# Performance work log

Measured on AMD Instinct MI355X. Metric: run time of the kernel, lower is better.

The kernel has to match this reference:

```python
import jax, jax.numpy as jnp
import numpy as np

# dims: N batch, O out_channels, CI in_channels, H=W vertices, R rank
N, O, CI, H, R = 8, 32, 16, 512, 8


def setup_inputs() -> dict:
    key = jax.random.key(0)
    kx, kw, kb = jax.random.split(key, 3)
    X = jax.random.normal(kx, (N, CI, H, H), dtype=jnp.float32)
    # learnable left generator (right generator aliases it under symmetry=True)
    weight_L = jax.random.normal(kw, (O, CI, H, R), dtype=jnp.float32) * 0.02
    fan_in = CI * H * R  # torch fan_in for a (O, CI, H, R) weight
    bound = 1.0 / np.sqrt(fan_in)
    bias = jax.random.uniform(kb, (O,), dtype=jnp.float32, minval=-bound, maxval=bound)
    # coupling='split': fixed (non-learnable) +/-1 diagonal coupling, first O//2 channels negative
    coupling = jnp.ones((O, CI, R, 1), dtype=jnp.float32).at[: O // 2].multiply(-1.0)
    return {"X": X, "weight_L": weight_L, "bias": bias, "coupling": coupling}


def reference(X, weight_L, bias, coupling):
    # --- template expansion: T[o,c] = L diag(coupling) L^T  (symmetric, low-rank) ---
    # coupling: (O,CI,R,1) -> per-rank sign broadcast over the rank axis of L
    Lc = weight_L * coupling[..., 0][..., None, :]            # (O,CI,H,R)
    T = jnp.einsum('ochr,ocwr->ochw', Lc, weight_L)           # (O,CI,H,W)
    # --- crosshair similarity, with the in_channel sum pulled inside ---
    P = jnp.einsum('nchw,ochw->nohw', X, T)                   # (N,O,H,W)
    out = P.sum(-1, keepdims=True) + P.sum(-2, keepdims=True) - P
    out = out + bias[None, :, None, None]
    # --- delete diagonal ---
    eye = jnp.eye(out.shape[-1], dtype=out.dtype)
    return out * (1.0 - eye)
```

## Files before the change

kernel.cpp:

```cpp
#include <hip/hip_runtime.h>
#include <cstdint>
#include <cstddef>
#include <utility>

#define Ndim 8
#define Odim 32
#define Cdim 16
#define Hdim 512
#define Rdim 8
#define TW 64
#define TH 4
#define NBW (Hdim/TW)
#define NBH (Hdim/TH)
#define HHsz ((size_t)Hdim*Hdim)

typedef _Float16 half2_t __attribute__((ext_vector_type(2)));
typedef unsigned int u32x4 __attribute__((ext_vector_type(4)));

union U16 { u32x4 u; half2_t h[4]; };

template <class F, int... Is>
__device__ __forceinline__ void unroll_impl(F&& f, std::integer_sequence<int, Is...>) {
    (f(std::integral_constant<int, Is>{}), ...);
}
template <int N, class F>
__device__ __forceinline__ void unrollN(F&& f) {
    unroll_impl(static_cast<F&&>(f), std::make_integer_sequence<int, N>{});
}

__device__ __forceinline__ half2_t pk(float a, float b) {
    half2_t h; h[0] = (_Float16)a; h[1] = (_Float16)b; return h;
}

#if defined(__has_builtin)
#if __has_builtin(__builtin_amdgcn_fdot2)
#define HAVE_FDOT2 1
#endif
#endif

__device__ __forceinline__ float fdot2f(half2_t a, half2_t b, float acc) {
#ifdef HAVE_FDOT2
    return __builtin_amdgcn_fdot2(a, b, acc, false);
#else
    return acc + (float)a[0] * (float)b[0] + (float)a[1] * (float)b[1];
#endif
}

__device__ __forceinline__ void stage16(const u32x4* g, u32x4* l) {
    __builtin_amdgcn_global_load_lds(
        (const __attribute__((address_space(1))) uint32_t*)g,
        (__attribute__((address_space(3))) uint32_t*)l, 16, 0, 0);
}

template<int CTRL>
__device__ __forceinline__ float dppadd(float v) {
    return v + __int_as_float(__builtin_amdgcn_update_dpp(
        0, __float_as_int(v), CTRL, 0xf, 0xf, true));
}
__device__ __forceinline__ float wave_sum63(float v) {
    v = dppadd<0xB1>(v);
    v = dppadd<0x4E>(v);
    v = dppadd<0x141>(v);
    v = dppadd<0x140>(v);
    v = dppadd<0x142>(v);
    v = dppadd<0x143>(v);
    return v;
}

__global__ __launch_bounds__(256)
void sylo_prep(const float* __restrict__ L, const float* __restrict__ coup,
               u32x4* __restrict__ lsigT, u32x4* __restrict__ lraw)
{
    int row = blockIdx.x * 256 + threadIdx.x;
    int oc = row >> 9, h = row & 511;
    int o = oc >> 4, c = oc & 15;
    const float4* lp = (const float4*)(L + (size_t)row * Rdim);
    const float4* cp = (const float4*)(coup + (size_t)oc * Rdim);
    float4 l0 = lp[0], l1 = lp[1];
    float4 c0 = cp[0], c1 = cp[1];
    U16 s, r;
    s.h[0] = pk(l0.x * c0.x, l0.y * c0.y); s.h[1] = pk(l0.z * c0.z, l0.w * c0.w);
    s.h[2] = pk(l1.x * c1.x, l1.y * c1.y); s.h[3] = pk(l1.z * c1.z, l1.w * c1.w);
    r.h[0] = pk(l0.x, l0.y); r.h[1] = pk(l0.z, l0.w);
    r.h[2] = pk(l1.x, l1.y); r.h[3] = pk(l1.z, l1.w);
    lsigT[((size_t)o * Hdim + h) * Cdim + c] = s.u;
    lraw[row] = r.u;
}

__global__ __launch_bounds__(256)
void sylo_xprep(const float* __restrict__ X, u32x4* __restrict__ Xh)
{
    int cid = blockIdx.x * 256 + threadIdx.x;
    int pxl = cid & 63;
    int k = (cid >> 6) & 15;
    size_t px = (size_t)(cid >> 10) * 64 + pxl;
    U16 v;
    unrollN<4>([&](auto ii) {
        constexpr int i = decltype(ii)::value;
        int pr = 4 * k + i;
        int cp = pr >> 3, n = pr & 7;
        float a = X[(size_t)(n * Cdim + 2 * cp)     * HHsz + px];
        float b = X[(size_t)(n * Cdim + 2 * cp + 1) * HHsz + px];
        v.h[i] = pk(a, b);
    });
    Xh[cid] = v.u;
}

template<int XH>
__device__ __forceinline__ void load_x(U16 (&xr)[16], const u32x4* __restrict__ Xh,
                                       const float* __restrict__ Xg,
                                       int hh, int bw, int j)
{
    if constexpr (XH) {
        const size_t base = ((size_t)hh * NBW + bw) * 1024 + j;
        unrollN<16>([&](auto ki) {
            constexpr int k = decltype(ki)::value;
            xr[k].u = Xh[base + k * 64];
        });
    } else {
        const size_t q = (size_t)hh * Hdim + bw * TW + j;
        unrollN<8>([&](auto cpi) {
            constexpr int cp = decltype(cpi)::value;
            unrollN<8>([&](auto ni) {
                constexpr int n = decltype(ni)::value;
                constexpr int idx = cp * 8 + n;
                xr[idx >> 2].h[idx & 3] = pk(Xg[(size_t)(n * Cdim + 2 * cp) * HHsz + q],
                                             Xg[(size_t)(n * Cdim + 2 * cp + 1) * HHsz + q]);
            });
            __builtin_amdgcn_sched_barrier(0);
        });
    }
    asm volatile("" :
        "+v"(xr[0].u), "+v"(xr[1].u), "+v"(xr[2].u), "+v"(xr[3].u),
        "+v"(xr[4].u), "+v"(xr[5].u), "+v"(xr[6].u), "+v"(xr[7].u),
        "+v"(xr[8].u), "+v"(xr[9].u), "+v"(xr[10].u), "+v"(xr[11].u),
        "+v"(xr[12].u), "+v"(xr[13].u), "+v"(xr[14].u), "+v"(xr[15].u));
}

__device__ __forceinline__ void stage_tile(const u32x4* __restrict__ lraw, int o,
                                           int w0, int j, int iw, u32x4 (&buf)[Cdim][TW])
{
    unrollN<4>([&](auto ki) {
        constexpr int k = decltype(ki)::value;
        int c = iw * 4 + k;
        stage16(lraw + ((size_t)(o * Cdim + c) * Hdim + w0 + j), &buf[c][0]);
    });
}
__device__ __forceinline__ void stage_tile_raw(const float* __restrict__ Lg, int o,
                                               int w0, int tid, u32x4 (&buf)[Cdim][TW])
{
    unrollN<4>([&](auto ki) {
        constexpr int k = decltype(ki)::value;
        int e = tid + k * 256, c = e >> 6, w = e & 63;
        const float4* gp = (const float4*)(Lg + ((size_t)(o * Cdim + c) * Hdim + w0 + w) * Rdim);
        float4 l0 = gp[0], l1 = gp[1];
        U16 t;
        t.h[0] = pk(l0.x, l0.y); t.h[1] = pk(l0.z, l0.w);
        t.h[2] = pk(l1.x, l1.y); t.h[3] = pk(l1.z, l1.w);
        buf[c][w] = t.u;
    });
}

template<int LP>
__device__ __forceinline__ void compute_p(
    int o, int ruh, int j, const u32x4 (&lwb)[Cdim][TW],
    const u32x4* __restrict__ lsigT, const float* __restrict__ Lg,
    const float* __restrict__ coupg, const U16 (&xr)[16], float (&p)[Ndim])
{
    unrollN<8>([&](auto ni) { p[decltype(ni)::value] = 0.f; });
    unrollN<8>([&](auto cpi) {
        constexpr int cp = decltype(cpi)::value;
        float tv0 = 0.f, tv1 = 0.f;
        unrollN<2>([&](auto hi) {
            constexpr int hf = decltype(hi)::value;
            constexpr int c = 2 * cp + hf;
            U16 A, B;
            if constexpr (LP) {
                A.u = lsigT[((size_t)o * Hdim + ruh) * Cdim + c];
            } else {
                const float4* a0 = (const float4*)(Lg + ((size_t)(o * Cdim + c) * Hdim + ruh) * Rdim);
                const float4* cpp = (const float4*)(coupg + (size_t)(o * Cdim + c) * Rdim);
                float4 l0 = a0[0], l1 = a0[1];
                float4 c0 = cpp[0], c1 = cpp[1];
                A.h[0] = pk(l0.x * c0.x, l0.y * c0.y); A.h[1] = pk(l0.z * c0.z, l0.w * c0.w);
                A.h[2] = pk(l1.x * c1.x, l1.y * c1.y); A.h[3] = pk(l1.z * c1.z, l1.w * c1.w);
            }
            B.u = lwb[c][j];
            float t = 0.f;
            unrollN<4>([&](auto ri) {
                constexpr int r = decltype(ri)::value;
                t = fdot2f(A.h[r], B.h[r], t);
            });
            if constexpr (hf == 0) tv0 = t; else tv1 = t;
        });
        half2_t t2 = pk(tv0, tv1);
        unrollN<8>([&](auto ni) {
            constexpr int n = decltype(ni)::value;
            constexpr int idx = cp * 8 + n;
            p[n] = fdot2f(t2, xr[idx >> 2].h[idx & 3], p[n]);
        });
        if constexpr (cp == 1 || cp == 3 || cp == 5)
            __builtin_amdgcn_sched_barrier(0);
    });
}

template<int XH, int LP, int DET>
__global__ __launch_bounds__(256, 4)
void sylo_p0(const float* __restrict__ Xg, const float* __restrict__ Lg,
             const float* __restrict__ coupg,
             const u32x4* __restrict__ Xh, const u32x4* __restrict__ lsigT,
             const u32x4* __restrict__ lraw,
             float* __restrict__ rsp, float* __restrict__ csp,
             float* __restrict__ rs, float* __restrict__ cs)
{
    const int tid = threadIdx.x;
    const int j = tid & 63, iw = tid >> 6;
    const int bw = blockIdx.x, bh = blockIdx.y;
    const int w0 = bw * TW, h0 = bh * TH;
    const int hh = h0 + iw;
    const size_t S = (size_t)Ndim * Odim * Hdim;

    __shared__ __align__(16) u32x4 lw[2][Cdim][TW];
    __shared__ float csl[TH][Ndim][TW];

    U16 xr[16];
    load_x<XH>(xr, Xh, Xg, hh, bw, j);
    const int ruh = __builtin_amdgcn_readfirstlane(hh);

    if (LP) stage_tile(lraw, 0, w0, j, iw, lw[0]);
    __syncthreads();

    for (int o = 0; o < Odim; ++o) {
        const int cur = LP ? (o & 1) : 0;
        if (LP) {
            if (o + 1 < Odim) stage_tile(lraw, o + 1, w0, j, iw, lw[cur ^ 1]);
        } else {
            stage_tile_raw(Lg, o, w0, tid, lw[0]);
            __syncthreads();
        }

        float p[Ndim];
        compute_p<LP>(o, ruh, j, lw[cur], lsigT, Lg, coupg, xr, p);

        unrollN<8>([&](auto ni) {
            constexpr int n = decltype(ni)::value;
            float r = wave_sum63(p[n]);
            if (j == 63) {
                size_t i0 = (size_t)(n * Odim + o) * Hdim + hh;
                if (DET) rsp[(size_t)bw * S + i0] = r;
                else atomicAdd(&rs[i0], r);
            }
            csl[iw][n][j] = p[n];
        });
        __syncthreads();
        unrollN<2>([&](auto ki) {
            constexpr int k = decltype(ki)::value;
            int f = tid + k * 256;
            int n = f >> 6, jj = f & 63;
            float v = csl[0][n][jj] + csl[1][n][jj] + csl[2][n][jj] + csl[3][n][jj];
            size_t idx = (size_t)(n * Odim + o) * Hdim + w0 + jj;
            if (DET) csp[(size_t)bh * S + idx] = v;
            else atomicAdd(&cs[idx], v);
        });
        __syncthreads();
    }
}

template<int XH, int LP>
__global__ __launch_bounds__(256, 4)
void sylo_p1(const float* __restrict__ Xg, const float* __restrict__ Lg,
             const float* __restrict__ coupg, const float* __restrict__ biasg,
             const u32x4* __restrict__ Xh, const u32x4* __restrict__ lsigT,
             const u32x4* __restrict__ lraw,
             float* __restrict__ outg,
             const float* __restrict__ rs, const float* __restrict__ cs)
{
    const int tid = threadIdx.x;
    const int j = tid & 63, iw = tid >> 6;
    const int bw = blockIdx.x, bh = blockIdx.y;
    const int w0 = bw * TW, h0 = bh * TH;
    const int hh = h0 + iw, ww = w0 + j;

    __shared__ __align__(16) u32x4 lw[2][Cdim][TW];

    U16 xr[16];
    load_x<XH>(xr, Xh, Xg, hh, bw, j);
    const int ruh = __builtin_amdgcn_readfirstlane(hh);

    if (LP) stage_tile(lraw, 0, w0, j, iw, lw[0]);
    __syncthreads();

    for (int o = 0; o < Odim; ++o) {
        const int cur = LP ? (o & 1) : 0;
        if (LP) {
            if (o + 1 < Odim) stage_tile(lraw, o + 1, w0, j, iw, lw[cur ^ 1]);
        } else {
            stage_tile_raw(Lg, o, w0, tid, lw[0]);
            __syncthreads();
        }

        float p[Ndim];
        compute_p<LP>(o, ruh, j, lw[cur], lsigT, Lg, coupg, xr, p);

        float bb = biasg[o];
        unrollN<8>([&](auto ni) {
            constexpr int n = decltype(ni)::value;
            size_t i0 = (size_t)(n * Odim + o) * Hdim;
            float rv = rs[i0 + (size_t)ruh];
            float cv = cs[i0 + ww];
            float v = rv + cv - p[n] + bb;
            if (hh == ww) v = 0.f;
            outg[(i0 + hh) * Hdim + ww] = v;
        });
        __syncthreads();
    }
}

__global__ __launch_bounds__(256)
void sylo_reduce(const float* __restrict__ rsp, const float* __restrict__ csp,
                 float* __restrict__ rs, float* __restrict__ cs)
{
    int t = blockIdx.x * 256 + threadIdx.x;
    const size_t S = (size_t)Ndim * Odim * Hdim;
    float a = 0.f;
    #pragma unroll
    for (int k = 0; k < NBW; ++k) a += rsp[(size_t)k * S + t];
    rs[t] = a;
    float b = 0.f;
    #pragma unroll 16
    for (int k = 0; k < NBH; ++k) b += csp[(size_t)k * S + t];
    cs[t] = b;
}

extern "C" void kernel_launch(void* const* d_in, const int* in_sizes, int n_in,
                              void* d_out, int out_size, void* d_ws, size_t ws_size,
                              hipStream_t stream)
{
    const float* X    = (const float*)d_in[0];
    const float* L    = (const float*)d_in[1];
    const float* bias = (const float*)d_in[2];
    const float* coup = (const float*)d_in[3];
    float* out = (float*)d_out;

    const size_t S    = (size_t)Ndim * Odim * Hdim;
    const size_t NL16 = (size_t)Odim * Cdim * Hdim;
    const size_t NXH  = HHsz * 16;
    const size_t need0 = NL16 * 16 * 2 + NXH * 16 + (size_t)(NBW + NBH) * S * 4 + 2 * S * 4;
    const size_t need1 = NL16 * 16 * 2 + NXH * 16 + 2 * S * 4;
    dim3 grid(NBW, NBH), blk(256);

    if (ws_size >= need0) {
        u32x4* lsigT = (u32x4*)d_ws;
        u32x4* lraw  = lsigT + NL16;
        u32x4* Xh    = lraw + NL16;
        float* rsp = (float*)(Xh + NXH);
        float* csp = rsp + (size_t)NBW * S;
        float* rs  = csp + (size_t)NBH * S;
        float* cs  = rs + S;
        sylo_prep<<<dim3(1024), blk, 0, stream>>>(L, coup, lsigT, lraw);
        sylo_xprep<<<dim3(16384), blk, 0, stream>>>(X, Xh);
        sylo_p0<1,1,1><<<grid, blk, 0, stream>>>(X, L, coup, Xh, lsigT, lraw, rsp, csp, rs, cs);
        sylo_reduce<<<dim3(512), blk, 0, stream>>>(rsp, csp, rs, cs);
        sylo_p1<1,1><<<grid, blk, 0, stream>>>(X, L, coup, bias, Xh, lsigT, lraw, out, rs, cs);
    } else if (ws_size >= need1) {
        u32x4* lsigT = (u32x4*)d_ws;
        u32x4* lraw  = lsigT + NL16;
        u32x4* Xh    = lraw + NL16;
        float* rs = (float*)(Xh + NXH);
        float* cs = rs + S;
        hipMemsetAsync(rs, 0, 2 * S * sizeof(float), stream);
        sylo_prep<<<dim3(1024), blk, 0, stream>>>(L, coup, lsigT, lraw);
        sylo_xprep<<<dim3(16384), blk, 0, stream>>>(X, Xh);
        sylo_p0<1,1,0><<<grid, blk, 0, stream>>>(X, L, coup, Xh, lsigT, lraw, nullptr, nullptr, rs, cs);
        sylo_p1<1,1><<<grid, blk, 0, stream>>>(X, L, coup, bias, Xh, lsigT, lraw, out, rs, cs);
    } else {
        float* rs = (float*)d_ws;
        float* cs = rs + S;
        hipMemsetAsync(rs, 0, 2 * S * sizeof(float), stream);
        sylo_p0<0,0,0><<<grid, blk, 0, stream>>>(X, L, coup, nullptr, nullptr, nullptr, nullptr, nullptr, rs, cs);
        sylo_p1<0,0><<<grid, blk, 0, stream>>>(X, L, coup, bias, nullptr, nullptr, nullptr, out, rs, cs);
    }
}
```

Baseline: 322.2 us.

## Store fp16 P from first pass and replace recompute pass with streaming epilogue

The first pass now writes the per-pixel P values, packed to fp16 with round-toward-zero conversion, into a workspace buffer. A simple streaming kernel then reads them back to build the output, so the second pass no longer recomputes P. The separate X-prep kernel is folded into the first pass, which writes a block-local fp16 X layout that is reused while iterating over output channels. The deterministic partial-sum reduction path is dropped in favour of atomics. In exchange the code adds a large extra fp16 write and read of P, rounds P to fp16 before the final subtraction, and makes the row and column sums non-deterministic.

```diff
diff --git a/kernel.cpp b/kernel.cpp
--- a/kernel.cpp
+++ b/kernel.cpp
@@ -15,9 +15,11 @@
 #define HHsz ((size_t)Hdim*Hdim)
 
 typedef _Float16 half2_t __attribute__((ext_vector_type(2)));
+typedef __fp16 fp16x2_t __attribute__((ext_vector_type(2)));
 typedef unsigned int u32x4 __attribute__((ext_vector_type(4)));
 
 union U16 { u32x4 u; half2_t h[4]; };
+union UPK { fp16x2_t f; half2_t h; unsigned int u; };
 
 template <class F, int... Is>
 __device__ __forceinline__ void unroll_impl(F&& f, std::integer_sequence<int, Is...>) {
@@ -33,10 +35,22 @@
 }
 
 #if defined(__has_builtin)
+#if __has_builtin(__builtin_amdgcn_cvt_pkrtz)
+#define HAVE_PKRTZ 1
+#endif
 #if __has_builtin(__builtin_amdgcn_fdot2)
 #define HAVE_FDOT2 1
 #endif
 #endif
+
+__device__ __forceinline__ half2_t pkz(float a, float b) {
+#ifdef HAVE_PKRTZ
+    UPK u; u.f = __builtin_amdgcn_cvt_pkrtz(a, b);
+    return u.h;
+#else
+    return pk(a, b);
+#endif
+}
 
 __device__ __forceinline__ float fdot2f(half2_t a, half2_t b, float acc) {
 #ifdef HAVE_FDOT2
@@ -87,56 +101,6 @@
     lraw[row] = r.u;
 }
 
-__global__ __launch_bounds__(256)
-void sylo_xprep(const float* __restrict__ X, u32x4* __restrict__ Xh)
-{
-    int cid = blockIdx.x * 256 + threadIdx.x;
-    int pxl = cid & 63;
-    int k = (cid >> 6) & 15;
-    size_t px = (size_t)(cid >> 10) * 64 + pxl;
-    U16 v;
-    unrollN<4>([&](auto ii) {
-        constexpr int i = decltype(ii)::value;
-        int pr = 4 * k + i;
-        int cp = pr >> 3, n = pr & 7;
-        float a = X[(size_t)(n * Cdim + 2 * cp)     * HHsz + px];
-        float b = X[(size_t)(n * Cdim + 2 * cp + 1) * HHsz + px];
-        v.h[i] = pk(a, b);
-    });
-    Xh[cid] = v.u;
-}
-
-template<int XH>
-__device__ __forceinline__ void load_x(U16 (&xr)[16], const u32x4* __restrict__ Xh,
-                                       const float* __restrict__ Xg,
-                                       int hh, int bw, int j)
-{
-    if constexpr (XH) {
-        const size_t base = ((size_t)hh * NBW + bw) * 1024 + j;
-        unrollN<16>([&](auto ki) {
-            constexpr int k = decltype(ki)::value;
-            xr[k].u = Xh[base + k * 64];
-        });
-    } else {
-        const size_t q = (size_t)hh * Hdim + bw * TW + j;
-        unrollN<8>([&](auto cpi) {
-            constexpr int cp = decltype(cpi)::value;
-            unrollN<8>([&](auto ni) {
-                constexpr int n = decltype(ni)::value;
-                constexpr int idx = cp * 8 + n;
-                xr[idx >> 2].h[idx & 3] = pk(Xg[(size_t)(n * Cdim + 2 * cp) * HHsz + q],
-                                             Xg[(size_t)(n * Cdim + 2 * cp + 1) * HHsz + q]);
-            });
-            __builtin_amdgcn_sched_barrier(0);
-        });
-    }
-    asm volatile("" :
-        "+v"(xr[0].u), "+v"(xr[1].u), "+v"(xr[2].u), "+v"(xr[3].u),
-        "+v"(xr[4].u), "+v"(xr[5].u), "+v"(xr[6].u), "+v"(xr[7].u),
-        "+v"(xr[8].u), "+v"(xr[9].u), "+v"(xr[10].u), "+v"(xr[11].u),
-        "+v"(xr[12].u), "+v"(xr[13].u), "+v"(xr[14].u), "+v"(xr[15].u));
-}
-
 __device__ __forceinline__ void stage_tile(const u32x4* __restrict__ lraw, int o,
                                            int w0, int j, int iw, u32x4 (&buf)[Cdim][TW])
 {
@@ -161,15 +125,31 @@
     });
 }
 
-template<int LP>
-__device__ __forceinline__ void compute_p(
-    int o, int ruh, int j, const u32x4 (&lwb)[Cdim][TW],
+template<int XH, int LP>
+__device__ __forceinline__ void compute_core(
+    int o, int ruh, int j, int tid,
+    const u32x4 (&lwb)[Cdim][TW], const u32x4* xsl,
+    const float* __restrict__ Xg, size_t q,
     const u32x4* __restrict__ lsigT, const float* __restrict__ Lg,
-    const float* __restrict__ coupg, const U16 (&xr)[16], float (&p)[Ndim])
+    const float* __restrict__ coupg, float (&p)[Ndim])
 {
     unrollN<8>([&](auto ni) { p[decltype(ni)::value] = 0.f; });
+    unsigned xofs = 0;
+    if constexpr (XH) { asm volatile("" : "+v"(xofs)); }
     unrollN<8>([&](auto cpi) {
         constexpr int cp = decltype(cpi)::value;
+        U16 x0, x1;
+        if constexpr (XH) {
+            x0.u = xsl[xofs + (2 * cp) * 256 + tid];
+            x1.u = xsl[xofs + (2 * cp + 1) * 256 + tid];
+        } else {
+            unrollN<4>([&](auto ni) { constexpr int n = decltype(ni)::value;
+                x0.h[n] = pk(Xg[(size_t)(n * Cdim + 2 * cp) * HHsz + q],
+                             Xg[(size_t)(n * Cdim + 2 * cp + 1) * HHsz + q]); });
+            unrollN<4>([&](auto ni) { constexpr int n = decltype(ni)::value;
+                x1.h[n] = pk(Xg[(size_t)((n + 4) * Cdim + 2 * cp) * HHsz + q],
+                             Xg[(size_t)((n + 4) * Cdim + 2 * cp + 1) * HHsz + q]); });
+        }
         float tv0 = 0.f, tv1 = 0.f;
         unrollN<2>([&](auto hi) {
             constexpr int hf = decltype(hi)::value;
@@ -194,62 +174,84 @@
             if constexpr (hf == 0) tv0 = t; else tv1 = t;
         });
         half2_t t2 = pk(tv0, tv1);
-        unrollN<8>([&](auto ni) {
-            constexpr int n = decltype(ni)::value;
-            constexpr int idx = cp * 8 + n;
-            p[n] = fdot2f(t2, xr[idx >> 2].h[idx & 3], p[n]);
-        });
+        unrollN<4>([&](auto ni) { constexpr int n = decltype(ni)::value;
+            p[n] = fdot2f(t2, x0.h[n], p[n]); });
+        unrollN<4>([&](auto ni) { constexpr int n = decltype(ni)::value;
+            p[n + 4] = fdot2f(t2, x1.h[n], p[n + 4]); });
         if constexpr (cp == 1 || cp == 3 || cp == 5)
             __builtin_amdgcn_sched_barrier(0);
     });
 }
 
-template<int XH, int LP, int DET>
+template<int BXH, int XH, int LP, int PF>
 __global__ __launch_bounds__(256, 4)
 void sylo_p0(const float* __restrict__ Xg, const float* __restrict__ Lg,
              const float* __restrict__ coupg,
-             const u32x4* __restrict__ Xh, const u32x4* __restrict__ lsigT,
-             const u32x4* __restrict__ lraw,
-             float* __restrict__ rsp, float* __restrict__ csp,
-             float* __restrict__ rs, float* __restrict__ cs)
+             const u32x4* __restrict__ lsigT, const u32x4* __restrict__ lraw,
+             u32x4* __restrict__ xh, u32x4* __restrict__ pf,
+             float* __restrict__ rs, float* __restrict__ cs,
+             int obase, int ocount)
 {
     const int tid = threadIdx.x;
     const int j = tid & 63, iw = tid >> 6;
     const int bw = blockIdx.x, bh = blockIdx.y;
-    const int w0 = bw * TW, h0 = bh * TH;
-    const int hh = h0 + iw;
-    const size_t S = (size_t)Ndim * Odim * Hdim;
+    const int w0 = bw * TW;
+    const int hh = bh * TH + iw, ww = w0 + j;
+    const size_t q = (size_t)hh * Hdim + ww;
 
     __shared__ __align__(16) u32x4 lw[2][Cdim][TW];
     __shared__ float csl[TH][Ndim][TW];
 
-    U16 xr[16];
-    load_x<XH>(xr, Xh, Xg, hh, bw, j);
+    u32x4* xsl = nullptr;
+    if constexpr (XH) xsl = xh + (size_t)(bh * NBW + bw) * 4096;
+
+    if constexpr (BXH) {
+        unrollN<16>([&](auto ki) {
+            constexpr int k = decltype(ki)::value;
+            U16 v;
+            unrollN<4>([&](auto ii) {
+                constexpr int i = decltype(ii)::value;
+                constexpr int pr = 4 * k + i;
+                constexpr int cp = pr >> 3, n = pr & 7;
+                v.h[i] = pk(Xg[(size_t)(n * Cdim + 2 * cp) * HHsz + q],
+                            Xg[(size_t)(n * Cdim + 2 * cp + 1) * HHsz + q]);
+            });
+            xsl[k * 256 + tid] = v.u;
+            if constexpr (k == 3 || k == 7 || k == 11) __builtin_amdgcn_sched_barrier(0);
+        });
+    }
+
     const int ruh = __builtin_amdgcn_readfirstlane(hh);
 
-    if (LP) stage_tile(lraw, 0, w0, j, iw, lw[0]);
+    if (LP) stage_tile(lraw, obase, w0, j, iw, lw[0]);
     __syncthreads();
 
-    for (int o = 0; o < Odim; ++o) {
-        const int cur = LP ? (o & 1) : 0;
+    for (int oo = 0; oo < ocount; ++oo) {
+        const int o = obase + oo;
+        const int cur = LP ? (oo & 1) : 0;
         if (LP) {
-            if (o + 1 < Odim) stage_tile(lraw, o + 1, w0, j, iw, lw[cur ^ 1]);
+            if (oo + 1 < ocount) stage_tile(lraw, o + 1, w0, j, iw, lw[cur ^ 1]);
         } else {
             stage_tile_raw(Lg, o, w0, tid, lw[0]);
             __syncthreads();
         }
 
         float p[Ndim];
-        compute_p<LP>(o, ruh, j, lw[cur], lsigT, Lg, coupg, xr, p);
+        compute_core<XH, LP>(o, ruh, j, tid, lw[cur], xsl, Xg, q, lsigT, Lg, coupg, p);
+
+        if constexpr (PF) {
+            U16 pv;
+            unrollN<4>([&](auto ki) {
+                constexpr int k = decltype(ki)::value;
+                pv.h[k] = pkz(p[2 * k], p[2 * k + 1]);
+            });
+            pf[((size_t)oo * Hdim + hh) * Hdim + ww] = pv.u;
+        }
 
         unrollN<8>([&](auto ni) {
             constexpr int n = decltype(ni)::value;
             float r = wave_sum63(p[n]);
-            if (j == 63) {
-                size_t i0 = (size_t)(n * Odim + o) * Hdim + hh;
-                if (DET) rsp[(size_t)bw * S + i0] = r;
-                else atomicAdd(&rs[i0], r);
-            }
+            if (j == 63) atomicAdd(&rs[(size_t)(n * Odim + o) * Hdim + hh], r);
             csl[iw][n][j] = p[n];
         });
         __syncthreads();
@@ -258,78 +260,74 @@
             int f = tid + k * 256;
             int n = f >> 6, jj = f & 63;
             float v = csl[0][n][jj] + csl[1][n][jj] + csl[2][n][jj] + csl[3][n][jj];
-            size_t idx = (size_t)(n * Odim + o) * Hdim + w0 + jj;
-            if (DET) csp[(size_t)bh * S + idx] = v;
-            else atomicAdd(&cs[idx], v);
+            atomicAdd(&cs[(size_t)(n * Odim + o) * Hdim + w0 + jj], v);
         });
         __syncthreads();
     }
 }
 
-template<int XH, int LP>
-__global__ __launch_bounds__(256, 4)
-void sylo_p1(const float* __restrict__ Xg, const float* __restrict__ Lg,
-             const float* __restrict__ coupg, const float* __restrict__ biasg,
-             const u32x4* __restrict__ Xh, const u32x4* __restrict__ lsigT,
-             const u32x4* __restrict__ lraw,
-             float* __restrict__ outg,
-             const float* __restrict__ rs, const float* __restrict__ cs)
+__global__ __launch_bounds__(256)
+void sylo_p1s(const u32x4* __restrict__ pf, const float* __restrict__ rs,
+              const float* __restrict__ cs, const float* __restrict__ biasg,
+              float* __restrict__ outg, int obase, int OL)
 {
     const int tid = threadIdx.x;
     const int j = tid & 63, iw = tid >> 6;
     const int bw = blockIdx.x, bh = blockIdx.y;
-    const int w0 = bw * TW, h0 = bh * TH;
-    const int hh = h0 + iw, ww = w0 + j;
-
+    const int hh = bh * TH + iw, ww = bw * TW + j;
+    const int ruh = __builtin_amdgcn_readfirstlane(hh);
+
+    for (int oo = 0; oo < OL; ++oo) {
+        const int oc = blockIdx.z * OL + oo;
+        const int o = obase + oc;
+        U16 pv;
+        pv.u = pf[((size_t)oc * Hdim + hh) * Hdim + ww];
+        float bb = biasg[o];
+        unrollN<4>([&](auto ki) {
+            constexpr int k = decltype(ki)::value;
+            constexpr int n0 = 2 * k, n1 = 2 * k + 1;
+            float pa = (float)pv.h[k][0], pb = (float)pv.h[k][1];
+            size_t i0 = (size_t)(n0 * Odim + o) * Hdim;
+            size_t i1 = (size_t)(n1 * Odim + o) * Hdim;
+            float v0 = rs[i0 + (size_t)ruh] + cs[i0 + ww] - pa + bb;
+            float v1 = rs[i1 + (size_t)ruh] + cs[i1 + ww] - pb + bb;
+            if (hh == ww) { v0 = 0.f; v1 = 0.f; }
+            outg[(i0 + hh) * Hdim + ww] = v0;
+            outg[(i1 + hh) * Hdim + ww] = v1;
+        });
+    }
+}
+
+__global__ __launch_bounds__(256, 4)
+void sylo_p1r(const float* __restrict__ Xg, const float* __restrict__ Lg,
+              const float* __restrict__ coupg, const float* __restrict__ biasg,
+              float* __restrict__ outg,
+              const float* __restrict__ rs, const float* __restrict__ cs)
+{
+    const int tid = threadIdx.x;
+    const int j = tid & 63, iw = tid >> 6;
+    const int bw = blockIdx.x, bh = blockIdx.y;
+    const int w0 = bw * TW;
+    const int hh = bh * TH + iw, ww = w0 + j;
+    const size_t q = (size_t)hh * Hdim + ww;
     __shared__ __align__(16) u32x4 lw[2][Cdim][TW];
-
-    U16 xr[16];
-    load_x<XH>(xr, Xh, Xg, hh, bw, j);
     const int ruh = __builtin_amdgcn_readfirstlane(hh);
 
-    if (LP) stage_tile(lraw, 0, w0, j, iw, lw[0]);
-    __syncthreads();
-
     for (int o = 0; o < Odim; ++o) {
-        const int cur = LP ? (o & 1) : 0;
-        if (LP) {
-            if (o + 1 < Odim) stage_tile(lraw, o + 1, w0, j, iw, lw[cur ^ 1]);
-        } else {
-            stage_tile_raw(Lg, o, w0, tid, lw[0]);
-            __syncthreads();
-        }
-
+        __syncthreads();
+        stage_tile_raw(Lg, o, w0, tid, lw[0]);
+        __syncthreads();
         float p[Ndim];
-        compute_p<LP>(o, ruh, j, lw[cur], lsigT, Lg, coupg, xr, p);
-
+        compute_core<0, 0>(o, ruh, j, tid, lw[0], nullptr, Xg, q, nullptr, Lg, coupg, p);
         float bb = biasg[o];
         unrollN<8>([&](auto ni) {
             constexpr int n = decltype(ni)::value;
             size_t i0 = (size_t)(n * Odim + o) * Hdim;
-            float rv = rs[i0 + (size_t)ruh];
-            float cv = cs[i0 + ww];
-            float v = rv + cv - p[n] + bb;
+            float v = rs[i0 + (size_t)ruh] + cs[i0 + ww] - p[n] + bb;
             if (hh == ww) v = 0.f;
             outg[(i0 + hh) * Hdim + ww] = v;
         });
-        __syncthreads();
-    }
-}
-
-__global__ __launch_bounds__(256)
-void sylo_reduce(const float* __restrict__ rsp, const float* __restrict__ csp,
-                 float* __restrict__ rs, float* __restrict__ cs)
-{
-    int t = blockIdx.x * 256 + threadIdx.x;
-    const size_t S = (size_t)Ndim * Odim * Hdim;
-    float a = 0.f;
-    #pragma unroll
-    for (int k = 0; k < NBW; ++k) a += rsp[(size_t)k * S + t];
-    rs[t] = a;
-    float b = 0.f;
-    #pragma unroll 16
-    for (int k = 0; k < NBH; ++k) b += csp[(size_t)k * S + t];
-    cs[t] = b;
+    }
 }
 
 extern "C" void kernel_launch(void* const* d_in, const int* in_sizes, int n_in,
@@ -342,42 +340,50 @@
     const float* coup = (const float*)d_in[3];
     float* out = (float*)d_out;
 
-    const size_t S    = (size_t)Ndim * Odim * Hdim;
-    const size_t NL16 = (size_t)Odim * Cdim * Hdim;
-    const size_t NXH  = HHsz * 16;
-    const size_t need0 = NL16 * 16 * 2 + NXH * 16 + (size_t)(NBW + NBH) * S * 4 + 2 * S * 4;
-    const size_t need1 = NL16 * 16 * 2 + NXH * 16 + 2 * S * 4;
-    dim3 grid(NBW, NBH), blk(256);
-
-    if (ws_size >= need0) {
-        u32x4* lsigT = (u32x4*)d_ws;
-        u32x4* lraw  = lsigT + NL16;
-        u32x4* Xh    = lraw + NL16;
-        float* rsp = (float*)(Xh + NXH);
-        float* csp = rsp + (size_t)NBW * S;
-        float* rs  = csp + (size_t)NBH * S;
-        float* cs  = rs + S;
-        sylo_prep<<<dim3(1024), blk, 0, stream>>>(L, coup, lsigT, lraw);
-        sylo_xprep<<<dim3(16384), blk, 0, stream>>>(X, Xh);
-        sylo_p0<1,1,1><<<grid, blk, 0, stream>>>(X, L, coup, Xh, lsigT, lraw, rsp, csp, rs, cs);
-        sylo_reduce<<<dim3(512), blk, 0, stream>>>(rsp, csp, rs, cs);
-        sylo_p1<1,1><<<grid, blk, 0, stream>>>(X, L, coup, bias, Xh, lsigT, lraw, out, rs, cs);
-    } else if (ws_size >= need1) {
-        u32x4* lsigT = (u32x4*)d_ws;
-        u32x4* lraw  = lsigT + NL16;
-        u32x4* Xh    = lraw + NL16;
-        float* rs = (float*)(Xh + NXH);
+    const size_t S     = (size_t)Ndim * Odim * Hdim;
+    const size_t NL16  = (size_t)Odim * Cdim * Hdim;
+    const size_t NXH   = (size_t)1024 * 4096;
+    const size_t pfPerO = HHsz * 16;
+
+    int C = 0, XH = 0, LP = 0;
+    auto tier = [&](int xh_, int lp_) {
+        size_t base = (lp_ ? 2 * NL16 * 16 : 0) + (xh_ ? NXH * 16 : 0) + 2 * S * 4;
+        const int cands[6] = {32, 16, 8, 4, 2, 1};
+        for (int i = 0; i < 6; ++i)
+            if (ws_size >= base + (size_t)cands[i] * pfPerO) { C = cands[i]; XH = xh_; LP = lp_; return true; }
+        return false;
+    };
+    dim3 g(NBW, NBH), b(256);
+
+    if (tier(1, 1) || tier(0, 1) || tier(0, 0)) {
+        char* p = (char*)d_ws;
+        u32x4 *lsigT = nullptr, *lraw = nullptr, *xh = nullptr, *pf;
+        if (LP) { lsigT = (u32x4*)p; p += NL16 * 16; lraw = (u32x4*)p; p += NL16 * 16; }
+        if (XH) { xh = (u32x4*)p; p += NXH * 16; }
+        pf = (u32x4*)p; p += (size_t)C * pfPerO;
+        float* rs = (float*)p;
         float* cs = rs + S;
-        hipMemsetAsync(rs, 0, 2 * S * sizeof(float), stream);
-        sylo_prep<<<dim3(1024), blk, 0, stream>>>(L, coup, lsigT, lraw);
-        sylo_xprep<<<dim3(16384), blk, 0, stream>>>(X, Xh);
-        sylo_p0<1,1,0><<<grid, blk, 0, stream>>>(X, L, coup, Xh, lsigT, lraw, nullptr, nullptr, rs, cs);
-        sylo_p1<1,1><<<grid, blk, 0, stream>>>(X, L, coup, bias, Xh, lsigT, lraw, out, rs, cs);
+        (void)hipMemsetAsync(rs, 0, 2 * S * sizeof(float), stream);
+        if (LP) sylo_prep<<<dim3(1024), b, 0, stream>>>(L, coup, lsigT, lraw);
+
+        for (int ob = 0; ob < Odim; ob += C) {
+            if (XH) {
+                if (ob == 0) sylo_p0<1,1,1,1><<<g, b, 0, stream>>>(X, L, coup, lsigT, lraw, xh, pf, rs, cs, ob, C);
+                else         sylo_p0<0,1,1,1><<<g, b, 0, stream>>>(X, L, coup, lsigT, lraw, xh, pf, rs, cs, ob, C);
+            } else if (LP) {
+                sylo_p0<0,0,1,1><<<g, b, 0, stream>>>(X, L, coup, lsigT, lraw, nullptr, pf, rs, cs, ob, C);
+            } else {
+                sylo_p0<0,0,0,1><<<g, b, 0, stream>>>(X, L, coup, nullptr, nullptr, nullptr, pf, rs, cs, ob, C);
+            }
+            int OL = (C > 16) ? 16 : C;
+            dim3 g2(NBW, NBH, C / OL);
+            sylo_p1s<<<g2, b, 0, stream>>>(pf, rs, cs, bias, out, ob, OL);
+        }
     } else {
         float* rs = (float*)d_ws;
         float* cs = rs + S;
-        hipMemsetAsync(rs, 0, 2 * S * sizeof(float), stream);
-        sylo_p0<0,0,0><<<grid, blk, 0, stream>>>(X, L, coup, nullptr, nullptr, nullptr, nullptr, nullptr, rs, cs);
-        sylo_p1<0,0><<<grid, blk, 0, stream>>>(X, L, coup, bias, nullptr, nullptr, nullptr, out, rs, cs);
-    }
-}
+        (void)hipMemsetAsync(rs, 0, 2 * S * sizeof(float), stream);
+        sylo_p0<0,0,0,0><<<g, b, 0, stream>>>(X, L, coup, nullptr, nullptr, nullptr, nullptr, rs, cs, 0, Odim);
+        sylo_p1r<<<g, b, 0, stream>>>(X, L, coup, bias, out, rs, cs);
+    }
+}
```

Result: slower. 475.1 us (+47.5%).
